# Performance work log

Measured on AMD Instinct MI355X. Metric: run time of the kernel, lower is better.

The kernel has to match this reference:

```python
import jax, jax.numpy as jnp
import numpy as np


def setup_inputs() -> dict:
    key = jax.random.key(0)
    k1, k2 = jax.random.split(key)
    B, N, E, D = 8, 2048, 64, 128
    spatial_embedding = jax.random.normal(k1, (B, N, E), dtype=jnp.float32)
    z = jax.random.normal(k2, (B, N, D), dtype=jnp.float32)
    return {"spatial_embedding": spatial_embedding, "z": z}


def reference(spatial_embedding, z):
    # Pairwise squared L2 distance via ||a||^2 + ||b||^2 - 2 a.b
    # (same math as (e0-e1).norm(2,-1)**2, avoids [B,N,N,E] intermediate)
    sq = jnp.sum(spatial_embedding * spatial_embedding, axis=-1)  # [B,N]
    inner = jnp.einsum('bie,bje->bij', spatial_embedding, spatial_embedding)
    d2 = jnp.maximum(sq[:, :, None] + sq[:, None, :] - 2.0 * inner, 0.0)  # [B,N,N]
    sim = jnp.exp(-d2)
    attn = sim / jnp.sum(sim, axis=-1, keepdims=True)
    out = jnp.einsum('bij,bjd->bid', attn, z)
    return out
```

## Files before the change

### kernel.cpp

```cpp
#include <hip/hip_runtime.h>
#include <hip/hip_bf16.h>

#define BB 8
#define NN 2048
#define EE 64
#define DD 128
#define BN (BB * NN)

typedef __attribute__((ext_vector_type(8))) short short8v;
typedef __attribute__((ext_vector_type(4))) float float4v;

__device__ __forceinline__ short f2bf(float f) {
    __hip_bfloat16 h = __float2bfloat16(f);
    return *reinterpret_cast<short*>(&h);
}
__device__ __forceinline__ uint32_t pack2bf(float a, float b) {
    return (uint32_t)(uint16_t)f2bf(a) | ((uint32_t)(uint16_t)f2bf(b) << 16);
}

#define GLD16(gp, lp)                                                          \
    __builtin_amdgcn_global_load_lds(                                          \
        (const __attribute__((address_space(1))) void*)(gp),                   \
        (__attribute__((address_space(3))) void*)(lp), 16, 0, 0)
#define GLD4(gp, lp)                                                           \
    __builtin_amdgcn_global_load_lds(                                          \
        (const __attribute__((address_space(1))) void*)(gp),                   \
        (__attribute__((address_space(3))) void*)(lp), 4, 0, 0)

__global__ __launch_bounds__(256) void prep_kernel(const float* __restrict__ emb,
                                                   const float* __restrict__ z,
                                                   short* __restrict__ embq,
                                                   short* __restrict__ zq,
                                                   float* __restrict__ sq) {
    __shared__ float zl[64 * 129];
    const int bid = blockIdx.x;
    const int t = threadIdx.x;

    if (bid < 512) {
        int gid = bid * 256 + t;
        int s = gid & 63;
        int ke = (gid >> 6) & 1;
        int r16 = (gid >> 7) & 127;
        int b = gid >> 14;
        int i = r16 * 16 + (s & 15);
        int e0 = ke * 32 + ((s >> 4) & 3) * 8;
        const float4* src = reinterpret_cast<const float4*>(emb + ((size_t)(b * NN + i)) * EE + e0);
        float4 v0 = src[0], v1 = src[1];
        short8v o;
        o[0] = f2bf(v0.x); o[1] = f2bf(v0.y); o[2] = f2bf(v0.z); o[3] = f2bf(v0.w);
        o[4] = f2bf(v1.x); o[5] = f2bf(v1.y); o[6] = f2bf(v1.z); o[7] = f2bf(v1.w);
        *reinterpret_cast<short8v*>(embq + (size_t)gid * 8) = o;
    } else if (bid < 768) {
        int v = bid - 512;
        int b = v >> 5;
        int jt = v & 31;
        int jb = jt * 64;
#pragma unroll
        for (int k = 0; k < 8; ++k) {
            int idx = t + k * 256;
            int jl = idx >> 5, c4 = idx & 31;
            float4 w = reinterpret_cast<const float4*>(z + ((size_t)(b * NN + jb + jl)) * DD)[c4];
            float* p = &zl[jl * 129 + c4 * 4];
            p[0] = w.x; p[1] = w.y; p[2] = w.z; p[3] = w.w;
        }
        __syncthreads();
#pragma unroll
        for (int k = 0; k < 4; ++k) {
            int sid = t + k * 256;
            int blk = sid >> 6, s = sid & 63;
            int ktl = blk >> 3, nt = blk & 7;
            int d = nt * 16 + (s & 15);
            int jl = ktl * 32 + ((s >> 4) & 3) * 8;
            short8v o;
#pragma unroll
            for (int e = 0; e < 8; ++e) o[e] = f2bf(zl[(jl + e) * 129 + d]);
            *reinterpret_cast<short8v*>(zq + ((size_t)((b * 64 + jt * 2 + ktl) * 8 + nt) * 64 + s) * 8) = o;
        }
    } else {
        int v = bid - 768;
        int q = t & 15;
#pragma unroll
        for (int p = 0; p < 4; ++p) {
            int row = v * 64 + p * 16 + (t >> 4);
            float4 rv = reinterpret_cast<const float4*>(emb + (size_t)row * EE)[q];
            float a0 = __bfloat162float(__float2bfloat16(rv.x));
            float a1 = __bfloat162float(__float2bfloat16(rv.y));
            float a2 = __bfloat162float(__float2bfloat16(rv.z));
            float a3 = __bfloat162float(__float2bfloat16(rv.w));
            float s2 = a0 * a0 + a1 * a1 + a2 * a2 + a3 * a3;
#pragma unroll
            for (int off = 1; off < 16; off <<= 1) s2 += __shfl_xor(s2, off);
            if (q == 0) sq[row] = s2;
        }
    }
}

__global__ __launch_bounds__(256, 2) void attn_mfma(const short* __restrict__ embq,
                                                    const short* __restrict__ zq,
                                                    const float* __restrict__ sq,
                                                    float* __restrict__ outnum,
                                                    float* __restrict__ den,
                                                    int njs) {
    __shared__ short sU[4][2048];
    __shared__ int4 sEmbJ[2][512];
    __shared__ float sSqJ[2][4][64];

    const int t = threadIdx.x;
    const int bid = blockIdx.x;
    const int b = bid & 7;
    const int q = bid >> 3;
    const int it = q & 15;
    const int js = q >> 4;
    const int ib = it * 128;
    const int w = t >> 6;
    const int l = t & 63;
    const int g = (l >> 4) & 3;
    const int c = l & 15;

    const int4* embqI4 = (const int4*)embq;
    const short8v* zq8 = (const short8v*)zq;
    const float* sqB = sq + b * NN;

    const int ntiles = 32 / njs;
    const int jt0 = js * ntiles;
    const int jtEnd = jt0 + ntiles;

    int4* sUi = (int4*)&sU[0][0];

#define STAGE(buf, tile)                                                       \
    do {                                                                       \
        const int4* _sj = embqI4 + (size_t)(b * 128 + (tile) * 4) * 2 * 64;    \
        GLD16(_sj + t, &sEmbJ[buf][t]);                                        \
        GLD16(_sj + t + 256, &sEmbJ[buf][t + 256]);                            \
        GLD4(sqB + (tile) * 64 + l, &sSqJ[buf][w][0]);                         \
    } while (0)

    {
        const int4* srcI = embqI4 + (size_t)(b * 128 + it * 8) * 2 * 64;
#pragma unroll
        for (int k = 0; k < 4; ++k) GLD16(srcI + t + k * 256, sUi + t + k * 256);
    }
    STAGE(0, jt0);
    STAGE(1, jt0 + 1);
    asm volatile("s_waitcnt vmcnt(3)" ::: "memory");
    __builtin_amdgcn_s_barrier();
    __builtin_amdgcn_sched_barrier(0);

    short8v qkB[2][2];
#pragma unroll
    for (int m = 0; m < 2; ++m)
#pragma unroll
        for (int ke = 0; ke < 2; ++ke)
            qkB[m][ke] = *reinterpret_cast<const short8v*>(&sUi[((w * 2 + m) * 2 + ke) * 64 + l]);
    float sqi[2];
#pragma unroll
    for (int m = 0; m < 2; ++m) sqi[m] = sqB[ib + w * 32 + m * 16 + c];

    float dsum[2] = {0.f, 0.f};
    float4v acc[2][8];
#pragma unroll
    for (int m = 0; m < 2; ++m)
#pragma unroll
        for (int nt = 0; nt < 8; ++nt) acc[m][nt] = (float4v){0.f, 0.f, 0.f, 0.f};

    char* ptw = (char*)&sU[w][0];
    const int swz = (c & 7) << 4;

    int cur = 0;
    for (int jt = jt0; jt < jtEnd; ++jt, cur ^= 1) {
        float d2v[2][4][4];
        float d2minJ[4];
#pragma unroll
        for (int J = 0; J < 4; ++J) {
            short8v a0 = *reinterpret_cast<const short8v*>(&sEmbJ[cur][(J * 2 + 0) * 64 + l]);
            short8v a1 = *reinterpret_cast<const short8v*>(&sEmbJ[cur][(J * 2 + 1) * 64 + l]);
            float4 sqj = *reinterpret_cast<const float4*>(&sSqJ[cur][w][J * 16 + 4 * g]);
            float mn = 1e30f;
#pragma unroll
            for (int m = 0; m < 2; ++m) {
                float4v sfr = (float4v){0.f, 0.f, 0.f, 0.f};
                sfr = __builtin_amdgcn_mfma_f32_16x16x32_bf16(a0, qkB[m][0], sfr, 0, 0, 0);
                sfr = __builtin_amdgcn_mfma_f32_16x16x32_bf16(a1, qkB[m][1], sfr, 0, 0, 0);
                d2v[m][J][0] = fmaxf(fmaf(-2.0f, sfr[0], sqi[m] + sqj.x), 0.0f);
                d2v[m][J][1] = fmaxf(fmaf(-2.0f, sfr[1], sqi[m] + sqj.y), 0.0f);
                d2v[m][J][2] = fmaxf(fmaf(-2.0f, sfr[2], sqi[m] + sqj.z), 0.0f);
                d2v[m][J][3] = fmaxf(fmaf(-2.0f, sfr[3], sqi[m] + sqj.w), 0.0f);
                mn = fminf(mn, fminf(fminf(d2v[m][J][0], d2v[m][J][1]),
                                     fminf(d2v[m][J][2], d2v[m][J][3])));
            }
            d2minJ[J] = mn;
        }
        float tmin = fminf(fminf(d2minJ[0], d2minJ[1]), fminf(d2minJ[2], d2minJ[3]));

        if (!__all(tmin > 13.8f)) {
#pragma unroll
            for (int J = 0; J < 4; ++J) {
                const bool live = !__all(d2minJ[J] > 13.8f);
#pragma unroll
                for (int m = 0; m < 2; ++m) {
                    unsigned long long pword = 0ull;
                    if (live) {
                        float p0 = __expf(-d2v[m][J][0]);
                        float p1 = __expf(-d2v[m][J][1]);
                        float p2 = __expf(-d2v[m][J][2]);
                        float p3 = __expf(-d2v[m][J][3]);
                        dsum[m] += (p0 + p1) + (p2 + p3);
                        pword = (unsigned long long)pack2bf(p0, p1) |
                                ((unsigned long long)pack2bf(p2, p3) << 32);
                    }
                    *reinterpret_cast<unsigned long long*>(
                        ptw + ((m * 2048 + c * 128 + g * 8) ^ swz ^ (J * 32))) = pword;
                }
            }
            short8v pa[2][2];
#pragma unroll
            for (int m = 0; m < 2; ++m)
#pragma unroll
                for (int kt = 0; kt < 2; ++kt)
                    pa[m][kt] = *reinterpret_cast<const short8v*>(
                        ptw + ((m * 2048 + c * 128 + kt * 64 + g * 16) ^ swz));
#pragma unroll
            for (int nt = 0; nt < 8; ++nt) {
                short8v z0 = zq8[(size_t)((b * 64 + jt * 2 + 0) * 8 + nt) * 64 + l];
                short8v z1 = zq8[(size_t)((b * 64 + jt * 2 + 1) * 8 + nt) * 64 + l];
#pragma unroll
                for (int m = 0; m < 2; ++m) {
                    acc[m][nt] = __builtin_amdgcn_mfma_f32_16x16x32_bf16(pa[m][0], z0, acc[m][nt], 0, 0, 0);
                    acc[m][nt] = __builtin_amdgcn_mfma_f32_16x16x32_bf16(pa[m][1], z1, acc[m][nt], 0, 0, 0);
                }
            }
        }

        __builtin_amdgcn_s_barrier();
        if (jt + 2 < jtEnd) {
            STAGE(cur, jt + 2);
            asm volatile("s_waitcnt vmcnt(3)" ::: "memory");
        } else {
            asm volatile("s_waitcnt vmcnt(0)" ::: "memory");
        }
        __builtin_amdgcn_s_barrier();
        __builtin_amdgcn_sched_barrier(0);
    }
#undef STAGE

#pragma unroll
    for (int m = 0; m < 2; ++m) {
        dsum[m] += __shfl_xor(dsum[m], 16);
        dsum[m] += __shfl_xor(dsum[m], 32);
    }

    if (njs == 1) {
#pragma unroll
        for (int m = 0; m < 2; ++m) {
            float invr[4];
#pragma unroll
            for (int r = 0; r < 4; ++r) invr[r] = 1.0f / __shfl(dsum[m], 4 * g + r);
#pragma unroll
            for (int r = 0; r < 4; ++r) {
                size_t row = (size_t)(b * NN + ib + w * 32 + m * 16 + 4 * g + r);
#pragma unroll
                for (int nt = 0; nt < 8; ++nt)
                    outnum[row * DD + nt * 16 + c] = acc[m][nt][r] * invr[r];
            }
        }
    } else {
        if (l < 16) {
            den[(size_t)js * BN + b * NN + ib + w * 32 + l] = dsum[0];
            den[(size_t)js * BN + b * NN + ib + w * 32 + 16 + l] = dsum[1];
        }
        if (!__all(fmaxf(dsum[0], dsum[1]) < 1e-6f)) {
#pragma unroll
            for (int m = 0; m < 2; ++m)
#pragma unroll
                for (int r = 0; r < 4; ++r) {
                    size_t row = (size_t)js * BN + b * NN + ib + w * 32 + m * 16 + 4 * g + r;
#pragma unroll
                    for (int nt = 0; nt < 8; ++nt)
                        outnum[row * DD + nt * 16 + c] = acc[m][nt][r];
                }
        }
    }
}

__global__ __launch_bounds__(256) void reduce_kernel(const float4* __restrict__ num,
                                                     const float* __restrict__ den,
                                                     float4* __restrict__ out,
                                                     int njs) {
    int i4 = blockIdx.x * 256 + threadIdx.x;
    int row = i4 >> 5;
    float4 ns = make_float4(0.f, 0.f, 0.f, 0.f);
    float ds = 0.f;
    for (int js = 0; js < njs; ++js) {
        float dj = den[(size_t)js * BN + row];
        ds += dj;
        if (dj >= 1e-6f) {
            float4 v = num[(size_t)js * ((size_t)BN * (DD / 4)) + i4];
            ns.x += v.x; ns.y += v.y; ns.z += v.z; ns.w += v.w;
        }
    }
    float inv = 1.0f / ds;
    out[i4] = make_float4(ns.x * inv, ns.y * inv, ns.z * inv, ns.w * inv);
}

extern "C" void kernel_launch(void* const* d_in, const int* in_sizes, int n_in,
                              void* d_out, int out_size, void* d_ws, size_t ws_size,
                              hipStream_t stream) {
    (void)in_sizes; (void)n_in; (void)out_size;
    const float* emb = (const float*)d_in[0];
    const float* z = (const float*)d_in[1];
    float* out = (float*)d_out;
    float* ws = (float*)d_ws;

    int njs = 1;
    if (ws_size >= 40ull * 1024 * 1024) njs = 4;
    else if (ws_size >= 24ull * 1024 * 1024) njs = 2;

    float* sqw = ws;
    float* denw = ws + BN;
    float* numw = denw + (size_t)njs * BN;
    size_t numFloats = (njs > 1) ? (size_t)njs * BN * DD : 0;
    short* embqw = (short*)(numw + numFloats);
    short* zqw = embqw + (size_t)BB * NN * EE;

    prep_kernel<<<1024, 256, 0, stream>>>(emb, z, embqw, zqw, sqw);

    attn_mfma<<<8 * 16 * njs, 256, 0, stream>>>(embqw, zqw, sqw,
                                                njs == 1 ? out : numw, denw, njs);

    if (njs > 1) {
        reduce_kernel<<<(BN * (DD / 4)) / 256, 256, 0, stream>>>(
            (const float4*)numw, denw, (float4*)out, njs);
    }
}
```

Measured before the change: 30.98 us.

## Load key tiles directly from global memory, dropping LDS staging and barriers

Removes the double-buffered global_load_lds staging of key embeddings and squared norms along with its per-tile block barriers. Each wave now reads its key fragments and norms straight from global memory (L1/L2) into registers every tile, and the query fragments are loaded directly as well. The per-tile skip test is restructured to decide liveness per 16-column subtile inline, which shortens register lifetimes. This removes synchronisation overhead, but each of the four waves now fetches the same key data redundantly and there is no explicit prefetch, so load latency may be exposed.

```diff
diff --git a/kernel.cpp b/kernel.cpp
--- a/kernel.cpp
+++ b/kernel.cpp
@@ -17,15 +17,6 @@
 __device__ __forceinline__ uint32_t pack2bf(float a, float b) {
     return (uint32_t)(uint16_t)f2bf(a) | ((uint32_t)(uint16_t)f2bf(b) << 16);
 }
-
-#define GLD16(gp, lp)                                                          \
-    __builtin_amdgcn_global_load_lds(                                          \
-        (const __attribute__((address_space(1))) void*)(gp),                   \
-        (__attribute__((address_space(3))) void*)(lp), 16, 0, 0)
-#define GLD4(gp, lp)                                                           \
-    __builtin_amdgcn_global_load_lds(                                          \
-        (const __attribute__((address_space(1))) void*)(gp),                   \
-        (__attribute__((address_space(3))) void*)(lp), 4, 0, 0)
 
 __global__ __launch_bounds__(256) void prep_kernel(const float* __restrict__ emb,
                                                    const float* __restrict__ z,
@@ -102,8 +93,6 @@
                                                     float* __restrict__ den,
                                                     int njs) {
     __shared__ short sU[4][2048];
-    __shared__ int4 sEmbJ[2][512];
-    __shared__ float sSqJ[2][4][64];
 
     const int t = threadIdx.x;
     const int bid = blockIdx.x;
@@ -117,7 +106,7 @@
     const int g = (l >> 4) & 3;
     const int c = l & 15;
 
-    const int4* embqI4 = (const int4*)embq;
+    const short8v* embq8 = (const short8v*)embq;
     const short8v* zq8 = (const short8v*)zq;
     const float* sqB = sq + b * NN;
 
@@ -125,33 +114,12 @@
     const int jt0 = js * ntiles;
     const int jtEnd = jt0 + ntiles;
 
-    int4* sUi = (int4*)&sU[0][0];
-
-#define STAGE(buf, tile)                                                       \
-    do {                                                                       \
-        const int4* _sj = embqI4 + (size_t)(b * 128 + (tile) * 4) * 2 * 64;    \
-        GLD16(_sj + t, &sEmbJ[buf][t]);                                        \
-        GLD16(_sj + t + 256, &sEmbJ[buf][t + 256]);                            \
-        GLD4(sqB + (tile) * 64 + l, &sSqJ[buf][w][0]);                         \
-    } while (0)
-
-    {
-        const int4* srcI = embqI4 + (size_t)(b * 128 + it * 8) * 2 * 64;
-#pragma unroll
-        for (int k = 0; k < 4; ++k) GLD16(srcI + t + k * 256, sUi + t + k * 256);
-    }
-    STAGE(0, jt0);
-    STAGE(1, jt0 + 1);
-    asm volatile("s_waitcnt vmcnt(3)" ::: "memory");
-    __builtin_amdgcn_s_barrier();
-    __builtin_amdgcn_sched_barrier(0);
-
     short8v qkB[2][2];
 #pragma unroll
     for (int m = 0; m < 2; ++m)
 #pragma unroll
         for (int ke = 0; ke < 2; ++ke)
-            qkB[m][ke] = *reinterpret_cast<const short8v*>(&sUi[((w * 2 + m) * 2 + ke) * 64 + l]);
+            qkB[m][ke] = embq8[((size_t)(b * 128 + it * 8 + w * 2 + m) * 2 + ke) * 64 + l];
     float sqi[2];
 #pragma unroll
     for (int m = 0; m < 2; ++m) sqi[m] = sqB[ib + w * 32 + m * 16 + c];
@@ -166,52 +134,52 @@
     char* ptw = (char*)&sU[w][0];
     const int swz = (c & 7) << 4;
 
-    int cur = 0;
-    for (int jt = jt0; jt < jtEnd; ++jt, cur ^= 1) {
-        float d2v[2][4][4];
-        float d2minJ[4];
+    for (int jt = jt0; jt < jtEnd; ++jt) {
+        short8v a[4][2];
+        float4 sqj[4];
 #pragma unroll
         for (int J = 0; J < 4; ++J) {
-            short8v a0 = *reinterpret_cast<const short8v*>(&sEmbJ[cur][(J * 2 + 0) * 64 + l]);
-            short8v a1 = *reinterpret_cast<const short8v*>(&sEmbJ[cur][(J * 2 + 1) * 64 + l]);
-            float4 sqj = *reinterpret_cast<const float4*>(&sSqJ[cur][w][J * 16 + 4 * g]);
+            a[J][0] = embq8[((size_t)(b * 128 + jt * 4 + J) * 2 + 0) * 64 + l];
+            a[J][1] = embq8[((size_t)(b * 128 + jt * 4 + J) * 2 + 1) * 64 + l];
+            sqj[J] = *reinterpret_cast<const float4*>(sqB + jt * 64 + J * 16 + 4 * g);
+        }
+
+        bool anyLive = false;
+#pragma unroll
+        for (int J = 0; J < 4; ++J) {
+            float d2[2][4];
             float mn = 1e30f;
 #pragma unroll
             for (int m = 0; m < 2; ++m) {
                 float4v sfr = (float4v){0.f, 0.f, 0.f, 0.f};
-                sfr = __builtin_amdgcn_mfma_f32_16x16x32_bf16(a0, qkB[m][0], sfr, 0, 0, 0);
-                sfr = __builtin_amdgcn_mfma_f32_16x16x32_bf16(a1, qkB[m][1], sfr, 0, 0, 0);
-                d2v[m][J][0] = fmaxf(fmaf(-2.0f, sfr[0], sqi[m] + sqj.x), 0.0f);
-                d2v[m][J][1] = fmaxf(fmaf(-2.0f, sfr[1], sqi[m] + sqj.y), 0.0f);
-                d2v[m][J][2] = fmaxf(fmaf(-2.0f, sfr[2], sqi[m] + sqj.z), 0.0f);
-                d2v[m][J][3] = fmaxf(fmaf(-2.0f, sfr[3], sqi[m] + sqj.w), 0.0f);
-                mn = fminf(mn, fminf(fminf(d2v[m][J][0], d2v[m][J][1]),
-                                     fminf(d2v[m][J][2], d2v[m][J][3])));
-            }
-            d2minJ[J] = mn;
-        }
-        float tmin = fminf(fminf(d2minJ[0], d2minJ[1]), fminf(d2minJ[2], d2minJ[3]));
-
-        if (!__all(tmin > 13.8f)) {
-#pragma unroll
-            for (int J = 0; J < 4; ++J) {
-                const bool live = !__all(d2minJ[J] > 13.8f);
-#pragma unroll
-                for (int m = 0; m < 2; ++m) {
-                    unsigned long long pword = 0ull;
-                    if (live) {
-                        float p0 = __expf(-d2v[m][J][0]);
-                        float p1 = __expf(-d2v[m][J][1]);
-                        float p2 = __expf(-d2v[m][J][2]);
-                        float p3 = __expf(-d2v[m][J][3]);
-                        dsum[m] += (p0 + p1) + (p2 + p3);
-                        pword = (unsigned long long)pack2bf(p0, p1) |
-                                ((unsigned long long)pack2bf(p2, p3) << 32);
-                    }
-                    *reinterpret_cast<unsigned long long*>(
-                        ptw + ((m * 2048 + c * 128 + g * 8) ^ swz ^ (J * 32))) = pword;
+                sfr = __builtin_amdgcn_mfma_f32_16x16x32_bf16(a[J][0], qkB[m][0], sfr, 0, 0, 0);
+                sfr = __builtin_amdgcn_mfma_f32_16x16x32_bf16(a[J][1], qkB[m][1], sfr, 0, 0, 0);
+                d2[m][0] = fmaxf(fmaf(-2.0f, sfr[0], sqi[m] + sqj[J].x), 0.0f);
+                d2[m][1] = fmaxf(fmaf(-2.0f, sfr[1], sqi[m] + sqj[J].y), 0.0f);
+                d2[m][2] = fmaxf(fmaf(-2.0f, sfr[2], sqi[m] + sqj[J].z), 0.0f);
+                d2[m][3] = fmaxf(fmaf(-2.0f, sfr[3], sqi[m] + sqj[J].w), 0.0f);
+                mn = fminf(mn, fminf(fminf(d2[m][0], d2[m][1]), fminf(d2[m][2], d2[m][3])));
+            }
+            const bool live = !__all(mn > 13.8f);
+#pragma unroll
+            for (int m = 0; m < 2; ++m) {
+                unsigned long long pword = 0ull;
+                if (live) {
+                    float p0 = __expf(-d2[m][0]);
+                    float p1 = __expf(-d2[m][1]);
+                    float p2 = __expf(-d2[m][2]);
+                    float p3 = __expf(-d2[m][3]);
+                    dsum[m] += (p0 + p1) + (p2 + p3);
+                    pword = (unsigned long long)pack2bf(p0, p1) |
+                            ((unsigned long long)pack2bf(p2, p3) << 32);
                 }
-            }
+                *reinterpret_cast<unsigned long long*>(
+                    ptw + ((m * 2048 + c * 128 + g * 8) ^ swz ^ (J * 32))) = pword;
+            }
+            anyLive |= live;
+        }
+
+        if (anyLive) {
             short8v pa[2][2];
 #pragma unroll
             for (int m = 0; m < 2; ++m)
@@ -230,18 +198,7 @@
                 }
             }
         }
-
-        __builtin_amdgcn_s_barrier();
-        if (jt + 2 < jtEnd) {
-            STAGE(cur, jt + 2);
-            asm volatile("s_waitcnt vmcnt(3)" ::: "memory");
-        } else {
-            asm volatile("s_waitcnt vmcnt(0)" ::: "memory");
-        }
-        __builtin_amdgcn_s_barrier();
-        __builtin_amdgcn_sched_barrier(0);
-    }
-#undef STAGE
+    }
 
 #pragma unroll
     for (int m = 0; m < 2; ++m) {
```

Result: no change. 30.48 us (-1.6%).
